# Kernel optimization log

Hardware: AMD Instinct MI355X
Metric: run time of the kernel (lower is better)

Reference implementation:

```python
import jax, jax.numpy as jnp
import numpy as np

B, S, HH, WW = 256, 384, 12, 16
D = HH * WW          # 192, LSTM input dim
H = 100              # hidden_dim
C = 250              # output_dim (N_CLASSES)


def setup_inputs() -> dict:
    key = jax.random.key(0)
    k1, k2, k3, k4 = jax.random.split(key, 4)
    x = jax.random.normal(k1, (B, S, HH, WW), dtype=jnp.float32)
    # Glorot-ish scaling to keep the recurrence numerically tame
    W = jax.random.normal(k2, (D, 4 * H), dtype=jnp.float32) / np.sqrt(D)
    U = jax.random.normal(k3, (H, 4 * H), dtype=jnp.float32) / np.sqrt(H)
    b = jnp.zeros((4 * H,), dtype=jnp.float32)
    Wd = jax.random.normal(k4, (H, C), dtype=jnp.float32) / np.sqrt(H)
    bd = jnp.zeros((C,), dtype=jnp.float32)
    return {"x": x, "W": W, "U": U, "b": b, "Wd": Wd, "bd": bd}


def _lstm_last_hidden(x3, W, U, b):
    # x3: [B, S, D]. Keras gate order: i, f, c(g), o.
    pre = jnp.einsum('bsd,dk->sbk', x3, W) + b  # time-major [S, B, 4H]
    h0 = jnp.zeros((x3.shape[0], H), dtype=x3.dtype)
    c0 = jnp.zeros_like(h0)

    def step(carry, xt):
        h, c = carry
        z = xt + h @ U                      # [B, 4H]
        i = jax.nn.sigmoid(z[:, 0 * H:1 * H])
        f = jax.nn.sigmoid(z[:, 1 * H:2 * H])
        g = jnp.tanh(z[:, 2 * H:3 * H])
        o = jax.nn.sigmoid(z[:, 3 * H:4 * H])
        c_new = f * c + i * g
        h_new = o * jnp.tanh(c_new)
        return (h_new, c_new), None

    (hT, _), _ = jax.lax.scan(step, (h0, c0), pre)
    return hT  # [B, H] == out[:, -1, :] since return_sequences last step = final state


def reference(x, W, U, b, Wd, bd):
    b_, s_, hh_, ww_ = x.shape
    x3 = x.reshape(b_, s_, hh_ * ww_)
    hT = _lstm_last_hidden(x3, W, U, b)
    # Dropout layers are identity at inference (training=False)
    return hT @ Wd + bd  # [B, C] logits
```

## Files before the change

kernel.cpp:

```cpp
#include <hip/hip_runtime.h>
#include <cstdint>
#include <cstddef>

#define S_LEN 384
#define BATCH 256
#define DIM   192
#define HID   100
#define G4    400
#define NCLS  250

#define LOG2E  1.4426950408889634f
#define LOG2E2 2.8853900817779268f

typedef float    f32x4   __attribute__((ext_vector_type(4)));
typedef short    bf16x8  __attribute__((ext_vector_type(8)));
typedef _Float16 half2_t __attribute__((ext_vector_type(2)));
typedef _Float16 f16x4   __attribute__((ext_vector_type(4)));
typedef _Float16 f16x8   __attribute__((ext_vector_type(8)));

static __device__ __forceinline__ unsigned short f2bf(float f) {
    unsigned u = __float_as_uint(f);
    return (unsigned short)((u + 0x7FFFu + ((u >> 16) & 1u)) >> 16);
}

template<int CTRL>
static __device__ __forceinline__ float fdpp(float x) {
    return __int_as_float(
        __builtin_amdgcn_mov_dpp(__float_as_int(x), CTRL, 0xF, 0xF, true));
}
#define DPP_X1 0xB1
#define DPP_X2 0x4E

__global__ void prep(const float* __restrict__ W, const float* __restrict__ U,
                     unsigned short* __restrict__ Wt, half2_t* __restrict__ Ut2)
{
    int bid = blockIdx.x;
    if (bid < 300) {
        int i = bid * 256 + threadIdx.x;
        if (i >= G4 * DIM) return;
        int k = i / DIM, d = i - k * DIM;
        Wt[i] = f2bf(W[(size_t)d * G4 + k]);
    } else {
        int i = (bid - 300) * 256 + threadIdx.x;
        if (i >= G4 * 52) return;
        int col = i / 52, p = i - col * 52;
        int j0 = 2 * p, j1 = 2 * p + 1;
        half2_t v;
        v.x = (_Float16)(j0 < HID ? U[(size_t)j0 * G4 + col] : 0.0f);
        v.y = (_Float16)(j1 < HID ? U[(size_t)j1 * G4 + col] : 0.0f);
        Ut2[i] = v;
    }
}

__global__ __launch_bounds__(256, 2)
void gemm_pre(const float* __restrict__ x, const unsigned short* __restrict__ Wt,
              const float* __restrict__ bias, _Float16* __restrict__ preh,
              int s_start, int chunk)
{
    __shared__ unsigned int xs[64 * 100];
    __shared__ unsigned int wsh[400 * 20];

    const int t    = threadIdx.x;
    const int lane = t & 63;
    const int w    = t >> 6;
    const int nsb  = chunk >> 6;
    const int b    = blockIdx.x / nsb;
    const int sblk = blockIdx.x - b * nsb;
    const float* __restrict__ xb = x + ((size_t)b * S_LEN + s_start + sblk * 64) * DIM;

#pragma unroll
    for (int r = 0; r < 12; ++r) {
        int i = t + r * 256;
        int row = i / 48, c4 = i - row * 48;
        float4 v = ((const float4*)(xb + (size_t)row * DIM))[c4];
        xs[row * 100 + c4 * 2]     = (unsigned)f2bf(v.x) | ((unsigned)f2bf(v.y) << 16);
        xs[row * 100 + c4 * 2 + 1] = (unsigned)f2bf(v.z) | ((unsigned)f2bf(v.w) << 16);
    }

    const int m = lane & 15, q = lane >> 4;

    float bv[25];
#pragma unroll
    for (int ct = 0; ct < 25; ++ct) bv[ct] = bias[ct * 16 + m];

    f32x4 acc[25];
#pragma unroll
    for (int ct = 0; ct < 25; ++ct) acc[ct] = (f32x4){0.f, 0.f, 0.f, 0.f};

    for (int dc = 0; dc < 6; ++dc) {
        if (dc) __syncthreads();
#pragma unroll
        for (int r = 0; r < 7; ++r) {
            int i = t + r * 256;
            if (i < 1600) {
                int k = i >> 2, u4 = i & 3;
                uint4 v = *(const uint4*)(Wt + (size_t)k * DIM + dc * 32 + u4 * 8);
                *(uint4*)(wsh + k * 20 + u4 * 4) = v;
            }
        }
        __syncthreads();

        const unsigned short* xp = (const unsigned short*)xs
                                   + (16 * w + m) * 200 + dc * 32 + q * 8;
        bf16x8 af = *(const bf16x8*)xp;
#pragma unroll
        for (int ct = 0; ct < 25; ++ct) {
            const unsigned short* bp = (const unsigned short*)wsh
                                       + (ct * 16 + m) * 40 + q * 8;
            bf16x8 bf = *(const bf16x8*)bp;
            acc[ct] = __builtin_amdgcn_mfma_f32_16x16x32_bf16(af, bf, acc[ct], 0, 0, 0);
        }
    }

    _Float16* __restrict__ pb = preh + (size_t)b * G4 * chunk + (size_t)sblk * 64
                                + 16 * w + q * 4;
#pragma unroll
    for (int ct = 0; ct < 25; ++ct) {
        f16x4 v;
        v[0] = (_Float16)(acc[ct][0] + bv[ct]);
        v[1] = (_Float16)(acc[ct][1] + bv[ct]);
        v[2] = (_Float16)(acc[ct][2] + bv[ct]);
        v[3] = (_Float16)(acc[ct][3] + bv[ct]);
        *(f16x4*)(pb + (size_t)(ct * 16 + m) * chunk) = v;
    }
}

__global__ __launch_bounds__(448)
void lstm_scan(const _Float16* __restrict__ preh, const half2_t* __restrict__ Ut2,
               const float* __restrict__ Wd, const float* __restrict__ bd,
               float* __restrict__ out, float* __restrict__ state,
               int nsteps, int first, int last)
{
    __shared__ _Float16 h2[2][160];
    __shared__ __align__(16) float hf32[HID];

    const int b  = blockIdx.x;
    const int t  = threadIdx.x;
    const int jg = t & 3;
    const int nr = t >> 2;
    const int n  = (nr < HID) ? nr : HID - 1;
    const bool active = (nr < HID);
    const int col  = jg * HID + n;
    const int slot = (n / 26) * 40 + (n % 26);

    half2_t Uc[4][13];
#pragma unroll
    for (int qq = 0; qq < 4; ++qq) {
        const half2_t* up = Ut2 + (size_t)(qq * HID + n) * 52 + 13 * jg;
#pragma unroll
        for (int r = 0; r < 13; ++r) Uc[qq][r] = up[r];
    }

    if (t < 320) ((_Float16*)h2)[t] = (_Float16)0.f;
    float c;
    if (first) {
        c = 0.f;
        __syncthreads();
    } else {
        c = state[BATCH * HID + b * HID + n];
        __syncthreads();
        if (t < HID) h2[0][(t / 26) * 40 + (t % 26)] = (_Float16)state[b * HID + t];
        __syncthreads();
    }

    const _Float16* __restrict__ zp = preh + ((size_t)b * G4 + col) * nsteps;
    f16x4 zA = *(const f16x4*)zp;
    f16x4 zB = *(const f16x4*)(zp + 4);

    const float scale = (jg == 2) ? -LOG2E2 : -LOG2E;
    const float Aact  = (jg == 2) ? 2.0f : 1.0f;
    const float Bact  = (jg == 2) ? -1.0f : 0.0f;
    const bool b0 = (jg & 1) != 0, b1 = (jg & 2) != 0;

    float hn_last = 0.f;

    auto step = [&](float zin, int cur) {
        const _Float16* hb = &h2[cur][jg * 40];
        f16x8  hA  = *(const f16x8*)hb;
        f16x8  hB  = *(const f16x8*)(hb + 8);
        f16x8  hC  = *(const f16x8*)(hb + 16);
        half2_t hD = *(const half2_t*)(hb + 24);
        half2_t hp[13];
        hp[0]  = __builtin_shufflevector(hA, hA, 0, 1);
        hp[1]  = __builtin_shufflevector(hA, hA, 2, 3);
        hp[2]  = __builtin_shufflevector(hA, hA, 4, 5);
        hp[3]  = __builtin_shufflevector(hA, hA, 6, 7);
        hp[4]  = __builtin_shufflevector(hB, hB, 0, 1);
        hp[5]  = __builtin_shufflevector(hB, hB, 2, 3);
        hp[6]  = __builtin_shufflevector(hB, hB, 4, 5);
        hp[7]  = __builtin_shufflevector(hB, hB, 6, 7);
        hp[8]  = __builtin_shufflevector(hC, hC, 0, 1);
        hp[9]  = __builtin_shufflevector(hC, hC, 2, 3);
        hp[10] = __builtin_shufflevector(hC, hC, 4, 5);
        hp[11] = __builtin_shufflevector(hC, hC, 6, 7);
        hp[12] = hD;

        float p0 = 0.f, p1 = 0.f, p2 = 0.f, p3 = 0.f;
#pragma unroll
        for (int r = 0; r < 13; ++r) {
            p0 = __builtin_amdgcn_fdot2(Uc[0][r], hp[r], p0, false);
            p1 = __builtin_amdgcn_fdot2(Uc[1][r], hp[r], p1, false);
            p2 = __builtin_amdgcn_fdot2(Uc[2][r], hp[r], p2, false);
            p3 = __builtin_amdgcn_fdot2(Uc[3][r], hp[r], p3, false);
        }

        float sA = b0 ? p0 : p1;  float rA = fdpp<DPP_X1>(sA);
        float sB = b0 ? p2 : p3;  float rB = fdpp<DPP_X1>(sB);
        float r0 = (b0 ? p1 : p0) + rA;
        float r1 = (b0 ? p3 : p2) + rB;
        float sC = b1 ? r0 : r1;  float rC = fdpp<DPP_X2>(sC);
        float a  = (b1 ? r1 : r0) + rC + zin;

        float e = __builtin_amdgcn_exp2f(scale * a);
        float v = fmaf(Aact, __builtin_amdgcn_rcpf(1.0f + e), Bact);

        float q1 = fdpp<DPP_X1>(v);
        float q2 = fdpp<DPP_X2>(v);
        float q3 = fdpp<DPP_X2>(q1);

        c = fmaf(q1, c, v * q2);
        float ec = __builtin_amdgcn_exp2f(-LOG2E2 * c);
        float tc = fmaf(2.0f, __builtin_amdgcn_rcpf(1.0f + ec), -1.0f);
        float hn = q3 * tc;
        if (jg == 0 && active) h2[cur ^ 1][slot] = (_Float16)hn;
        hn_last = hn;
        __syncthreads();
    };

    for (int s4 = 0; s4 < nsteps; s4 += 4) {
        f16x4 zn = zA; zA = zB;
        if (s4 + 8 < nsteps) zB = *(const f16x4*)(zp + s4 + 8);
        step((float)zn[0], 0);
        step((float)zn[1], 1);
        step((float)zn[2], 0);
        step((float)zn[3], 1);
    }

    if (last) {
        if (jg == 0 && active) hf32[n] = hn_last;
        __syncthreads();
        if (t < NCLS) {
            float acc2 = bd[t];
            const float4* h4 = (const float4*)hf32;
#pragma unroll 5
            for (int j4 = 0; j4 < 25; ++j4) {
                float4 hv = h4[j4];
                acc2 = fmaf(hv.x, Wd[(size_t)(4 * j4 + 0) * NCLS + t], acc2);
                acc2 = fmaf(hv.y, Wd[(size_t)(4 * j4 + 1) * NCLS + t], acc2);
                acc2 = fmaf(hv.z, Wd[(size_t)(4 * j4 + 2) * NCLS + t], acc2);
                acc2 = fmaf(hv.w, Wd[(size_t)(4 * j4 + 3) * NCLS + t], acc2);
            }
            out[(size_t)b * NCLS + t] = acc2;
        }
    } else {
        if (jg == 0 && active) {
            state[b * HID + n] = hn_last;
            state[BATCH * HID + b * HID + n] = c;
        }
    }
}

extern "C" void kernel_launch(void* const* d_in, const int* in_sizes, int n_in,
                              void* d_out, int out_size, void* d_ws, size_t ws_size,
                              hipStream_t stream)
{
    const float* x    = (const float*)d_in[0];
    const float* W    = (const float*)d_in[1];
    const float* U    = (const float*)d_in[2];
    const float* bias = (const float*)d_in[3];
    const float* Wd   = (const float*)d_in[4];
    const float* bd   = (const float*)d_in[5];
    float* out = (float*)d_out;

    const size_t fixed_dw = 51200 + 20800 + 38400;
    int chunk = 64;
    if      (ws_size >= (fixed_dw + (size_t)384 * 51200) * 4) chunk = 384;
    else if (ws_size >= (fixed_dw + (size_t)192 * 51200) * 4) chunk = 192;
    const int nchunks = S_LEN / chunk;

    unsigned int* wsb = (unsigned int*)d_ws;
    float*          state = (float*)wsb;
    half2_t*        Ut2   = (half2_t*)(wsb + 51200);
    unsigned short* Wt    = (unsigned short*)(wsb + 72000);
    _Float16*       preh  = (_Float16*)(wsb + 110400);

    prep<<<382, 256, 0, stream>>>(W, U, Wt, Ut2);

    for (int ci = 0; ci < nchunks; ++ci) {
        const int s0 = ci * chunk;
        gemm_pre<<<BATCH * (chunk >> 6), 256, 0, stream>>>(x, Wt, bias, preh, s0, chunk);
        lstm_scan<<<BATCH, 448, 0, stream>>>(preh, Ut2, Wd, bd, out, state,
                                             chunk, ci == 0 ? 1 : 0,
                                             ci == nchunks - 1 ? 1 : 0);
    }
}
```

Baseline: 330.2 us.

## Load GEMM operands directly from global and simplify scan DPP reduction

The pre-activation GEMM no longer stages x and W tiles through shared memory with barriers. Each lane now loads its A fragment straight from global, converts it to bf16, and reads W fragments directly, relying on cache reuse. In the scan kernel the U register columns are permuted by jg so the cross-lane reduction needs no selects, and the z prefetch is widened to 16 steps per iteration. The risk is more redundant global and L2 traffic for W in the GEMM, plus higher register pressure from the deeper unroll.

New measurement: 404.0 us. 22.3% more time.

```diff
diff --git a/kernel.cpp b/kernel.cpp
--- a/kernel.cpp
+++ b/kernel.cpp
@@ -57,60 +57,42 @@
               const float* __restrict__ bias, _Float16* __restrict__ preh,
               int s_start, int chunk)
 {
-    __shared__ unsigned int xs[64 * 100];
-    __shared__ unsigned int wsh[400 * 20];
-
     const int t    = threadIdx.x;
     const int lane = t & 63;
     const int w    = t >> 6;
     const int nsb  = chunk >> 6;
     const int b    = blockIdx.x / nsb;
     const int sblk = blockIdx.x - b * nsb;
-    const float* __restrict__ xb = x + ((size_t)b * S_LEN + s_start + sblk * 64) * DIM;
-
-#pragma unroll
-    for (int r = 0; r < 12; ++r) {
-        int i = t + r * 256;
-        int row = i / 48, c4 = i - row * 48;
-        float4 v = ((const float4*)(xb + (size_t)row * DIM))[c4];
-        xs[row * 100 + c4 * 2]     = (unsigned)f2bf(v.x) | ((unsigned)f2bf(v.y) << 16);
-        xs[row * 100 + c4 * 2 + 1] = (unsigned)f2bf(v.z) | ((unsigned)f2bf(v.w) << 16);
-    }
-
     const int m = lane & 15, q = lane >> 4;
 
+    const float* __restrict__ xr =
+        x + ((size_t)b * S_LEN + s_start + sblk * 64 + 16 * w + m) * DIM + q * 8;
+    const unsigned short* __restrict__ wb = Wt + (size_t)m * DIM + q * 8;
+
+    f32x4 acc[25];
+#pragma unroll
+    for (int ct = 0; ct < 25; ++ct) acc[ct] = (f32x4){0.f, 0.f, 0.f, 0.f};
+
+#pragma unroll
+    for (int dc = 0; dc < 6; ++dc) {
+        float4 a0 = *(const float4*)(xr + dc * 32);
+        float4 a1 = *(const float4*)(xr + dc * 32 + 4);
+        bf16x8 af;
+        af[0] = (short)f2bf(a0.x); af[1] = (short)f2bf(a0.y);
+        af[2] = (short)f2bf(a0.z); af[3] = (short)f2bf(a0.w);
+        af[4] = (short)f2bf(a1.x); af[5] = (short)f2bf(a1.y);
+        af[6] = (short)f2bf(a1.z); af[7] = (short)f2bf(a1.w);
+        const unsigned short* __restrict__ wp = wb + dc * 32;
+#pragma unroll
+        for (int ct = 0; ct < 25; ++ct) {
+            bf16x8 bf = *(const bf16x8*)(wp + (size_t)ct * (16 * DIM));
+            acc[ct] = __builtin_amdgcn_mfma_f32_16x16x32_bf16(af, bf, acc[ct], 0, 0, 0);
+        }
+    }
+
     float bv[25];
 #pragma unroll
     for (int ct = 0; ct < 25; ++ct) bv[ct] = bias[ct * 16 + m];
-
-    f32x4 acc[25];
-#pragma unroll
-    for (int ct = 0; ct < 25; ++ct) acc[ct] = (f32x4){0.f, 0.f, 0.f, 0.f};
-
-    for (int dc = 0; dc < 6; ++dc) {
-        if (dc) __syncthreads();
-#pragma unroll
-        for (int r = 0; r < 7; ++r) {
-            int i = t + r * 256;
-            if (i < 1600) {
-                int k = i >> 2, u4 = i & 3;
-                uint4 v = *(const uint4*)(Wt + (size_t)k * DIM + dc * 32 + u4 * 8);
-                *(uint4*)(wsh + k * 20 + u4 * 4) = v;
-            }
-        }
-        __syncthreads();
-
-        const unsigned short* xp = (const unsigned short*)xs
-                                   + (16 * w + m) * 200 + dc * 32 + q * 8;
-        bf16x8 af = *(const bf16x8*)xp;
-#pragma unroll
-        for (int ct = 0; ct < 25; ++ct) {
-            const unsigned short* bp = (const unsigned short*)wsh
-                                       + (ct * 16 + m) * 40 + q * 8;
-            bf16x8 bf = *(const bf16x8*)bp;
-            acc[ct] = __builtin_amdgcn_mfma_f32_16x16x32_bf16(af, bf, acc[ct], 0, 0, 0);
-        }
-    }
 
     _Float16* __restrict__ pb = preh + (size_t)b * G4 * chunk + (size_t)sblk * 64
                                 + 16 * w + q * 4;
@@ -145,10 +127,11 @@
 
     half2_t Uc[4][13];
 #pragma unroll
-    for (int qq = 0; qq < 4; ++qq) {
+    for (int i = 0; i < 4; ++i) {
+        const int qq = jg ^ i;
         const half2_t* up = Ut2 + (size_t)(qq * HID + n) * 52 + 13 * jg;
 #pragma unroll
-        for (int r = 0; r < 13; ++r) Uc[qq][r] = up[r];
+        for (int r = 0; r < 13; ++r) Uc[i][r] = up[r];
     }
 
     if (t < 320) ((_Float16*)h2)[t] = (_Float16)0.f;
@@ -164,13 +147,12 @@
     }
 
     const _Float16* __restrict__ zp = preh + ((size_t)b * G4 + col) * nsteps;
-    f16x4 zA = *(const f16x4*)zp;
-    f16x4 zB = *(const f16x4*)(zp + 4);
+    f16x8 zA = *(const f16x8*)zp;
+    f16x8 zB = *(const f16x8*)(zp + 8);
 
     const float scale = (jg == 2) ? -LOG2E2 : -LOG2E;
     const float Aact  = (jg == 2) ? 2.0f : 1.0f;
     const float Bact  = (jg == 2) ? -1.0f : 0.0f;
-    const bool b0 = (jg & 1) != 0, b1 = (jg & 2) != 0;
 
     float hn_last = 0.f;
 
@@ -204,12 +186,9 @@
             p3 = __builtin_amdgcn_fdot2(Uc[3][r], hp[r], p3, false);
         }
 
-        float sA = b0 ? p0 : p1;  float rA = fdpp<DPP_X1>(sA);
-        float sB = b0 ? p2 : p3;  float rB = fdpp<DPP_X1>(sB);
-        float r0 = (b0 ? p1 : p0) + rA;
-        float r1 = (b0 ? p3 : p2) + rB;
-        float sC = b1 ? r0 : r1;  float rC = fdpp<DPP_X2>(sC);
-        float a  = (b1 ? r1 : r0) + rC + zin;
+        float r0 = p0 + fdpp<DPP_X1>(p1);
+        float r1 = p2 + fdpp<DPP_X1>(p3);
+        float a  = r0 + fdpp<DPP_X2>(r1) + zin;
 
         float e = __builtin_amdgcn_exp2f(scale * a);
         float v = fmaf(Aact, __builtin_amdgcn_rcpf(1.0f + e), Bact);
@@ -227,13 +206,16 @@
         __syncthreads();
     };
 
-    for (int s4 = 0; s4 < nsteps; s4 += 4) {
-        f16x4 zn = zA; zA = zB;
-        if (s4 + 8 < nsteps) zB = *(const f16x4*)(zp + s4 + 8);
-        step((float)zn[0], 0);
-        step((float)zn[1], 1);
-        step((float)zn[2], 0);
-        step((float)zn[3], 1);
+    for (int s16 = 0; s16 < nsteps; s16 += 16) {
+        f16x8 zc = zA, zd = zB;
+        if (s16 + 16 < nsteps) {
+            zA = *(const f16x8*)(zp + s16 + 16);
+            zB = *(const f16x8*)(zp + s16 + 24);
+        }
+#pragma unroll
+        for (int k = 0; k < 8; ++k) step((float)zc[k], k & 1);
+#pragma unroll
+        for (int k = 0; k < 8; ++k) step((float)zd[k], k & 1);
     }
 
     if (last) {
```

## Split LSTM scan work across 2 lanes per hidden unit instead of 4

Applied to the files above, without the earlier changes.

Changes the recurrent scan from four lanes per hidden unit (one per gate, each doing 13 dot2 over a quarter of h) to two lanes per hidden unit, each doing all four gates over half of h. The block shrinks from 448 to 256 threads (4 waves) and the reduction needs only one DPP exchange instead of a two-level swizzle. The U weights are re-laid out in prep to match. Fewer waves should make each per-step barrier cheaper and cut cross-lane shuffles, at the cost of twice the dot2 work and twice the U registers per thread, with less parallelism hiding latency.

New measurement: 321.8 us. 2.6% less time.

```diff
diff --git a/kernel.cpp b/kernel.cpp
--- a/kernel.cpp
+++ b/kernel.cpp
@@ -29,10 +29,9 @@
         __builtin_amdgcn_mov_dpp(__float_as_int(x), CTRL, 0xF, 0xF, true));
 }
 #define DPP_X1 0xB1
-#define DPP_X2 0x4E
 
 __global__ void prep(const float* __restrict__ W, const float* __restrict__ U,
-                     unsigned short* __restrict__ Wt, half2_t* __restrict__ Ut2)
+                     unsigned short* __restrict__ Wt, half2_t* __restrict__ Ut2b)
 {
     int bid = blockIdx.x;
     if (bid < 300) {
@@ -42,13 +41,20 @@
         Wt[i] = f2bf(W[(size_t)d * G4 + k]);
     } else {
         int i = (bid - 300) * 256 + threadIdx.x;
-        if (i >= G4 * 52) return;
-        int col = i / 52, p = i - col * 52;
-        int j0 = 2 * p, j1 = 2 * p + 1;
+        if (i >= 20800) return;
+        int n    = i / 208;
+        int rem  = i - n * 208;
+        int p    = rem / 104;
+        int rem2 = rem - p * 104;
+        int gi   = rem2 / 26;
+        int r    = rem2 - gi * 26;
+        int g    = (gi < 2) ? (2 * p + gi) : (2 * (1 - p) + (gi - 2));
+        int col  = g * HID + n;
+        int j0   = 52 * p + 2 * r;
         half2_t v;
-        v.x = (_Float16)(j0 < HID ? U[(size_t)j0 * G4 + col] : 0.0f);
-        v.y = (_Float16)(j1 < HID ? U[(size_t)j1 * G4 + col] : 0.0f);
-        Ut2[i] = v;
+        v.x = (_Float16)(j0     < HID ? U[(size_t)j0       * G4 + col] : 0.0f);
+        v.y = (_Float16)(j0 + 1 < HID ? U[(size_t)(j0 + 1) * G4 + col] : 0.0f);
+        Ut2b[i] = v;
     }
 }
 
@@ -125,33 +131,32 @@
     }
 }
 
-__global__ __launch_bounds__(448)
-void lstm_scan(const _Float16* __restrict__ preh, const half2_t* __restrict__ Ut2,
+__global__ __launch_bounds__(256)
+void lstm_scan(const _Float16* __restrict__ preh, const half2_t* __restrict__ Ut2b,
                const float* __restrict__ Wd, const float* __restrict__ bd,
                float* __restrict__ out, float* __restrict__ state,
                int nsteps, int first, int last)
 {
-    __shared__ _Float16 h2[2][160];
+    __shared__ __align__(16) _Float16 h2[2][112];
     __shared__ __align__(16) float hf32[HID];
 
     const int b  = blockIdx.x;
     const int t  = threadIdx.x;
-    const int jg = t & 3;
-    const int nr = t >> 2;
+    const int p  = t & 1;
+    const int nr = t >> 1;
     const int n  = (nr < HID) ? nr : HID - 1;
     const bool active = (nr < HID);
-    const int col  = jg * HID + n;
-    const int slot = (n / 26) * 40 + (n % 26);
-
-    half2_t Uc[4][13];
-#pragma unroll
-    for (int qq = 0; qq < 4; ++qq) {
-        const half2_t* up = Ut2 + (size_t)(qq * HID + n) * 52 + 13 * jg;
-#pragma unroll
-        for (int r = 0; r < 13; ++r) Uc[qq][r] = up[r];
-    }
-
-    if (t < 320) ((_Float16*)h2)[t] = (_Float16)0.f;
+    const int slot = (n < 52) ? n : (56 + n - 52);
+
+    half2_t Uc[4][26];
+#pragma unroll
+    for (int gi = 0; gi < 4; ++gi) {
+        const half2_t* up = Ut2b + (size_t)((n * 2 + p) * 4 + gi) * 26;
+#pragma unroll
+        for (int r = 0; r < 26; ++r) Uc[gi][r] = up[r];
+    }
+
+    if (t < 224) ((_Float16*)h2)[t] = (_Float16)0.f;
     float c;
     if (first) {
         c = 0.f;
@@ -159,85 +164,107 @@
     } else {
         c = state[BATCH * HID + b * HID + n];
         __syncthreads();
-        if (t < HID) h2[0][(t / 26) * 40 + (t % 26)] = (_Float16)state[b * HID + t];
-        __syncthreads();
-    }
-
-    const _Float16* __restrict__ zp = preh + ((size_t)b * G4 + col) * nsteps;
-    f16x4 zA = *(const f16x4*)zp;
-    f16x4 zB = *(const f16x4*)(zp + 4);
-
-    const float scale = (jg == 2) ? -LOG2E2 : -LOG2E;
-    const float Aact  = (jg == 2) ? 2.0f : 1.0f;
-    const float Bact  = (jg == 2) ? -1.0f : 0.0f;
-    const bool b0 = (jg & 1) != 0, b1 = (jg & 2) != 0;
+        if (t < HID) h2[0][(t < 52) ? t : (56 + t - 52)] = (_Float16)state[b * HID + t];
+        __syncthreads();
+    }
+
+    const _Float16* __restrict__ zpA = preh + ((size_t)b * G4 + (2 * p)     * HID + n) * nsteps;
+    const _Float16* __restrict__ zpB = preh + ((size_t)b * G4 + (2 * p + 1) * HID + n) * nsteps;
+
+    const float scaleA = p ? -LOG2E2 : -LOG2E;
+    const float AactA  = p ? 2.0f : 1.0f;
+    const float BactA  = p ? -1.0f : 0.0f;
 
     float hn_last = 0.f;
 
-    auto step = [&](float zin, int cur) {
-        const _Float16* hb = &h2[cur][jg * 40];
-        f16x8  hA  = *(const f16x8*)hb;
-        f16x8  hB  = *(const f16x8*)(hb + 8);
-        f16x8  hC  = *(const f16x8*)(hb + 16);
-        half2_t hD = *(const half2_t*)(hb + 24);
-        half2_t hp[13];
-        hp[0]  = __builtin_shufflevector(hA, hA, 0, 1);
-        hp[1]  = __builtin_shufflevector(hA, hA, 2, 3);
-        hp[2]  = __builtin_shufflevector(hA, hA, 4, 5);
-        hp[3]  = __builtin_shufflevector(hA, hA, 6, 7);
-        hp[4]  = __builtin_shufflevector(hB, hB, 0, 1);
-        hp[5]  = __builtin_shufflevector(hB, hB, 2, 3);
-        hp[6]  = __builtin_shufflevector(hB, hB, 4, 5);
-        hp[7]  = __builtin_shufflevector(hB, hB, 6, 7);
-        hp[8]  = __builtin_shufflevector(hC, hC, 0, 1);
-        hp[9]  = __builtin_shufflevector(hC, hC, 2, 3);
-        hp[10] = __builtin_shufflevector(hC, hC, 4, 5);
-        hp[11] = __builtin_shufflevector(hC, hC, 6, 7);
-        hp[12] = hD;
-
-        float p0 = 0.f, p1 = 0.f, p2 = 0.f, p3 = 0.f;
+    auto step = [&](float zAk, float zBk, int cur) {
+        const _Float16* hb = &h2[cur][p * 56];
+        f16x8  g0 = *(const f16x8*)(hb);
+        f16x8  g1 = *(const f16x8*)(hb + 8);
+        f16x8  g2 = *(const f16x8*)(hb + 16);
+        f16x8  g3 = *(const f16x8*)(hb + 24);
+        f16x8  g4 = *(const f16x8*)(hb + 32);
+        f16x8  g5 = *(const f16x8*)(hb + 40);
+        f16x4  g6 = *(const f16x4*)(hb + 48);
+        half2_t hp[26];
+        hp[0]  = __builtin_shufflevector(g0, g0, 0, 1);
+        hp[1]  = __builtin_shufflevector(g0, g0, 2, 3);
+        hp[2]  = __builtin_shufflevector(g0, g0, 4, 5);
+        hp[3]  = __builtin_shufflevector(g0, g0, 6, 7);
+        hp[4]  = __builtin_shufflevector(g1, g1, 0, 1);
+        hp[5]  = __builtin_shufflevector(g1, g1, 2, 3);
+        hp[6]  = __builtin_shufflevector(g1, g1, 4, 5);
+        hp[7]  = __builtin_shufflevector(g1, g1, 6, 7);
+        hp[8]  = __builtin_shufflevector(g2, g2, 0, 1);
+        hp[9]  = __builtin_shufflevector(g2, g2, 2, 3);
+        hp[10] = __builtin_shufflevector(g2, g2, 4, 5);
+        hp[11] = __builtin_shufflevector(g2, g2, 6, 7);
+        hp[12] = __builtin_shufflevector(g3, g3, 0, 1);
+        hp[13] = __builtin_shufflevector(g3, g3, 2, 3);
+        hp[14] = __builtin_shufflevector(g3, g3, 4, 5);
+        hp[15] = __builtin_shufflevector(g3, g3, 6, 7);
+        hp[16] = __builtin_shufflevector(g4, g4, 0, 1);
+        hp[17] = __builtin_shufflevector(g4, g4, 2, 3);
+        hp[18] = __builtin_shufflevector(g4, g4, 4, 5);
+        hp[19] = __builtin_shufflevector(g4, g4, 6, 7);
+        hp[20] = __builtin_shufflevector(g5, g5, 0, 1);
+        hp[21] = __builtin_shufflevector(g5, g5, 2, 3);
+        hp[22] = __builtin_shufflevector(g5, g5, 4, 5);
+        hp[23] = __builtin_shufflevector(g5, g5, 6, 7);
+        hp[24] = __builtin_shufflevector(g6, g6, 0, 1);
+        hp[25] = __builtin_shufflevector(g6, g6, 2, 3);
+
+        float qa0 = 0.f, qa1 = 0.f, qa2 = 0.f, qa3 = 0.f;
+        float qb0 = 0.f, qb1 = 0.f, qb2 = 0.f, qb3 = 0.f;
 #pragma unroll
         for (int r = 0; r < 13; ++r) {
-            p0 = __builtin_amdgcn_fdot2(Uc[0][r], hp[r], p0, false);
-            p1 = __builtin_amdgcn_fdot2(Uc[1][r], hp[r], p1, false);
-            p2 = __builtin_amdgcn_fdot2(Uc[2][r], hp[r], p2, false);
-            p3 = __builtin_amdgcn_fdot2(Uc[3][r], hp[r], p3, false);
-        }
-
-        float sA = b0 ? p0 : p1;  float rA = fdpp<DPP_X1>(sA);
-        float sB = b0 ? p2 : p3;  float rB = fdpp<DPP_X1>(sB);
-        float r0 = (b0 ? p1 : p0) + rA;
-        float r1 = (b0 ? p3 : p2) + rB;
-        float sC = b1 ? r0 : r1;  float rC = fdpp<DPP_X2>(sC);
-        float a  = (b1 ? r1 : r0) + rC + zin;
-
-        float e = __builtin_amdgcn_exp2f(scale * a);
-        float v = fmaf(Aact, __builtin_amdgcn_rcpf(1.0f + e), Bact);
-
-        float q1 = fdpp<DPP_X1>(v);
-        float q2 = fdpp<DPP_X2>(v);
-        float q3 = fdpp<DPP_X2>(q1);
-
-        c = fmaf(q1, c, v * q2);
-        float ec = __builtin_amdgcn_exp2f(-LOG2E2 * c);
-        float tc = fmaf(2.0f, __builtin_amdgcn_rcpf(1.0f + ec), -1.0f);
-        float hn = q3 * tc;
-        if (jg == 0 && active) h2[cur ^ 1][slot] = (_Float16)hn;
+            qa0 = __builtin_amdgcn_fdot2(Uc[0][r], hp[r], qa0, false);
+            qa1 = __builtin_amdgcn_fdot2(Uc[1][r], hp[r], qa1, false);
+            qa2 = __builtin_amdgcn_fdot2(Uc[2][r], hp[r], qa2, false);
+            qa3 = __builtin_amdgcn_fdot2(Uc[3][r], hp[r], qa3, false);
+        }
+#pragma unroll
+        for (int r = 13; r < 26; ++r) {
+            qb0 = __builtin_amdgcn_fdot2(Uc[0][r], hp[r], qb0, false);
+            qb1 = __builtin_amdgcn_fdot2(Uc[1][r], hp[r], qb1, false);
+            qb2 = __builtin_amdgcn_fdot2(Uc[2][r], hp[r], qb2, false);
+            qb3 = __builtin_amdgcn_fdot2(Uc[3][r], hp[r], qb3, false);
+        }
+        float a0 = qa0 + qb0;
+        float a1 = qa1 + qb1;
+        float a2 = qa2 + qb2;
+        float a3 = qa3 + qb3;
+
+        float aA = a0 + fdpp<DPP_X1>(a2) + zAk;
+        float aB = a1 + fdpp<DPP_X1>(a3) + zBk;
+
+        float vA = fmaf(AactA,
+                        __builtin_amdgcn_rcpf(1.0f + __builtin_amdgcn_exp2f(scaleA * aA)),
+                        BactA);
+        float vB = __builtin_amdgcn_rcpf(1.0f + __builtin_amdgcn_exp2f(-LOG2E * aB));
+        float gA = fdpp<DPP_X1>(vA);
+        float gB = fdpp<DPP_X1>(vB);
+
+        c = fmaf(vB, c, vA * gA);
+        float tc = fmaf(2.0f,
+                        __builtin_amdgcn_rcpf(1.0f + __builtin_amdgcn_exp2f(-LOG2E2 * c)),
+                        -1.0f);
+        float hn = gB * tc;
+        if (p == 0 && active) h2[cur ^ 1][slot] = (_Float16)hn;
         hn_last = hn;
         __syncthreads();
     };
 
-    for (int s4 = 0; s4 < nsteps; s4 += 4) {
-        f16x4 zn = zA; zA = zB;
-        if (s4 + 8 < nsteps) zB = *(const f16x4*)(zp + s4 + 8);
-        step((float)zn[0], 0);
-        step((float)zn[1], 1);
-        step((float)zn[2], 0);
-        step((float)zn[3], 1);
+    for (int s8 = 0; s8 < nsteps; s8 += 8) {
+        f16x8 zva = *(const f16x8*)(zpA + s8);
+        f16x8 zvb = *(const f16x8*)(zpB + s8);
+#pragma unroll
+        for (int k = 0; k < 8; ++k)
+            step((float)zva[k], (float)zvb[k], k & 1);
     }
 
     if (last) {
-        if (jg == 0 && active) hf32[n] = hn_last;
+        if (p == 0 && active) hf32[n] = hn_last;
         __syncthreads();
         if (t < NCLS) {
             float acc2 = bd[t];
@@ -253,7 +280,7 @@
             out[(size_t)b * NCLS + t] = acc2;
         }
     } else {
-        if (jg == 0 && active) {
+        if (p == 0 && active) {
             state[b * HID + n] = hn_last;
             state[BATCH * HID + b * HID + n] = c;
         }
@@ -280,16 +307,16 @@
 
     unsigned int* wsb = (unsigned int*)d_ws;
     float*          state = (float*)wsb;
-    half2_t*        Ut2   = (half2_t*)(wsb + 51200);
+    half2_t*        Ut2b  = (half2_t*)(wsb + 51200);
     unsigned short* Wt    = (unsigned short*)(wsb + 72000);
     _Float16*       preh  = (_Float16*)(wsb + 110400);
 
-    prep<<<382, 256, 0, stream>>>(W, U, Wt, Ut2);
+    prep<<<382, 256, 0, stream>>>(W, U, Wt, Ut2b);
 
     for (int ci = 0; ci < nchunks; ++ci) {
         const int s0 = ci * chunk;
         gemm_pre<<<BATCH * (chunk >> 6), 256, 0, stream>>>(x, Wt, bias, preh, s0, chunk);
-        lstm_scan<<<BATCH, 448, 0, stream>>>(preh, Ut2, Wd, bd, out, state,
+        lstm_scan<<<BATCH, 256, 0, stream>>>(preh, Ut2b, Wd, bd, out, state,
                                              chunk, ci == 0 ? 1 : 0,
                                              ci == nchunks - 1 ? 1 : 0);
     }
```
